# Kernel tuning notes

Measured on AMD Instinct MI355X. Metric: run time of the kernel, lower is better.

Reference implementation:

```python
import jax, jax.numpy as jnp
import numpy as np

B, T, F, H = 32, 1024, 128, 256
NUM_LAYERS = 3  # 2 return_sequences LSTMs + final LSTM


def setup_inputs() -> dict:
    key = jax.random.key(0)
    ks = jax.random.split(key, 2 + 3 * NUM_LAYERS + 2)
    x = jax.random.normal(ks[0], (B, 2, T, F), jnp.float32)
    # ragged lengths: pad tail with zeros (Masking(mask_value=0) semantics)
    lengths = jax.random.randint(ks[1], (B, 2), T // 4, T + 1)
    tmask = (jnp.arange(T)[None, None, :] < lengths[:, :, None]).astype(jnp.float32)
    x = x * tmask[..., None]
    inp = {"inputs": x}
    in_dims = [F] + [H] * (NUM_LAYERS - 1)
    for i, d in enumerate(in_dims):
        k = 2 + 3 * i
        inp[f"W{i}"] = jax.random.normal(ks[k], (d, 4 * H), jnp.float32) * (1.0 / np.sqrt(d))
        inp[f"U{i}"] = jax.random.normal(ks[k + 1], (H, 4 * H), jnp.float32) * (1.0 / np.sqrt(H))
        b = jnp.zeros((4 * H,), jnp.float32)
        inp[f"b{i}"] = b.at[H:2 * H].set(1.0)  # keras unit_forget_bias
    inp["dense_w"] = jax.random.normal(ks[-2], (1, 1), jnp.float32)
    inp["dense_b"] = jnp.zeros((1,), jnp.float32)
    return inp


def lstm_layer(x, mask, W, U, b):
    """Keras-style masked LSTM. x: [B,T,D], mask: [B,T] bool.
    Masked steps carry previous h/c and previous output (keras K.rnn masking).
    Gate order i,f,g,o; sigmoid recurrent activation, tanh activation."""
    xT = jnp.swapaxes(x, 0, 1)                  # [T,B,D]
    mT = jnp.swapaxes(mask, 0, 1)[..., None]    # [T,B,1]
    bsz, hd = x.shape[0], U.shape[0]
    h0 = jnp.zeros((bsz, hd), x.dtype)

    def step(carry, inp):
        h, c = carry
        x_t, m = inp
        z = x_t @ W + h @ U + b                 # [B,4H]
        i, f, g, o = jnp.split(z, 4, axis=-1)
        c_new = jax.nn.sigmoid(f) * c + jax.nn.sigmoid(i) * jnp.tanh(g)
        h_new = jax.nn.sigmoid(o) * jnp.tanh(c_new)
        h = jnp.where(m, h_new, h)
        c = jnp.where(m, c_new, c)
        return (h, c), h

    (h_final, _), ys = jax.lax.scan(step, (h0, h0), (xT, mT))
    return jnp.swapaxes(ys, 0, 1), h_final


def encode(x, Ws, Us, bs):
    mask = jnp.any(x != 0, axis=-1)             # Masking(mask_value=0)
    for W, U, b in zip(Ws[:-1], Us[:-1], bs[:-1]):
        x, _ = lstm_layer(x, mask, W, U, b)     # dropout is identity at inference
    _, h = lstm_layer(x, mask, Ws[-1], Us[-1], bs[-1])
    return h


def reference(inputs, W0, U0, b0, W1, U1, b1, W2, U2, b2, dense_w, dense_b):
    Ws, Us, bs = [W0, W1, W2], [U0, U1, U2], [b0, b1, b2]
    h1 = encode(inputs[:, 0], Ws, Us, bs)
    h2 = encode(inputs[:, 1], Ws, Us, bs)
    dist = jnp.linalg.norm(h1 - h2, axis=1, keepdims=True)   # [B,1]
    dist = jnp.clip(dist, 1e-7, 1e7)
    return jax.nn.sigmoid(dist @ dense_w + dense_b)          # [B,1]
```

## Files before the change

### kernel.cpp

```cpp
#include <hip/hip_runtime.h>


typedef __attribute__((ext_vector_type(8))) short bf16x8;
typedef __attribute__((ext_vector_type(4))) float f32x4;
typedef __attribute__((ext_vector_type(4))) unsigned int u32x4;
typedef unsigned long long ull;

__device__ __forceinline__ unsigned short f2bf(float f){
    unsigned u = __float_as_uint(f);
    u += 0x7FFFu + ((u >> 16) & 1u);
    return (unsigned short)(u >> 16);
}
__device__ __forceinline__ float fsig(float x){
    return __builtin_amdgcn_rcpf(1.0f + __expf(-x));
}
__device__ __forceinline__ float ftanh(float x){
    float e = __expf(-2.0f * fabsf(x));
    return copysignf((1.0f - e) * __builtin_amdgcn_rcpf(1.0f + e), x);
}
__device__ __forceinline__ ull ald(const ull* p){
    return __hip_atomic_load(p, __ATOMIC_RELAXED, __HIP_MEMORY_SCOPE_AGENT);
}
__device__ __forceinline__ void ast(unsigned int* p, unsigned int v){
    __hip_atomic_store(p, v, __ATOMIC_RELAXED, __HIP_MEMORY_SCOPE_AGENT);
}
__device__ __forceinline__ void st_pair(ull* p, ull v){
    asm volatile("global_store_dwordx2 %0, %1, off sc1" :: "v"((ull)p), "v"(v) : "memory");
}
__device__ __forceinline__ void st_plain(ull* p, ull v){
    asm volatile("global_store_dwordx2 %0, %1, off" :: "v"((ull)p), "v"(v) : "memory");
}
__device__ __forceinline__ int min16(const ull* p){
    int m = 0x7FFFFFFF;
    #pragma unroll
    for (int i = 0; i < 8; ++i){
        ull v = ald(p + i);
        m = min(m, min((int)(unsigned)v, (int)(v >> 32)));
    }
    return m;
}

#define POLL4_SC1(P, Q0,Q1,Q2,Q3)                                        \
  asm volatile("global_load_dwordx4 %0, %4, off sc1\n\t"                 \
               "global_load_dwordx4 %1, %4, off offset:1024 sc1\n\t"     \
               "global_load_dwordx4 %2, %4, off offset:2048 sc1\n\t"     \
               "global_load_dwordx4 %3, %4, off offset:3072 sc1"         \
               : "=&v"(Q0),"=&v"(Q1),"=&v"(Q2),"=&v"(Q3)                 \
               : "v"(P) : "memory")
#define POLL4_SC0(P, Q0,Q1,Q2,Q3)                                        \
  asm volatile("global_load_dwordx4 %0, %4, off sc0\n\t"                 \
               "global_load_dwordx4 %1, %4, off offset:1024 sc0\n\t"     \
               "global_load_dwordx4 %2, %4, off offset:2048 sc0\n\t"     \
               "global_load_dwordx4 %3, %4, off offset:3072 sc0"         \
               : "=&v"(Q0),"=&v"(Q1),"=&v"(Q2),"=&v"(Q3)                 \
               : "v"(P) : "memory")
#define PLAIN4(P, O0,O1,O2,O3)                                           \
  asm volatile("global_load_dwordx4 %0, %4, off\n\t"                     \
               "global_load_dwordx4 %1, %4, off offset:1024\n\t"         \
               "global_load_dwordx4 %2, %4, off offset:2048\n\t"         \
               "global_load_dwordx4 %3, %4, off offset:3072"             \
               : "=&v"(O0),"=&v"(O1),"=&v"(O2),"=&v"(O3)                 \
               : "v"(P) : "memory")

__device__ __forceinline__ ull pk(u32x4 q){
    return (((ull)(unsigned)q.z) << 32) | (unsigned)q.x;
}

template<bool FAST>
__device__ __forceinline__ void poll_tile(const char* tile, unsigned tg, int half,
                                          unsigned int* buf, int lane){
    const ull b0 = (ull)(tile + lane * 16 + half * 8192);
    u32x4 q0,q1,q2,q3,q4,q5,q6,q7;
    int spins = 0;
    for (;;){
        if (FAST){
            POLL4_SC0(b0,        q0, q1, q2, q3);
            POLL4_SC0(b0 + 4096, q4, q5, q6, q7);
        } else {
            POLL4_SC1(b0,        q0, q1, q2, q3);
            POLL4_SC1(b0 + 4096, q4, q5, q6, q7);
        }
        asm volatile("s_waitcnt vmcnt(0)" ::: "memory");
        __builtin_amdgcn_sched_barrier(0);
        bool ok = (q0.y==tg)&(q0.w==tg)&(q1.y==tg)&(q1.w==tg)
                & (q2.y==tg)&(q2.w==tg)&(q3.y==tg)&(q3.w==tg)
                & (q4.y==tg)&(q4.w==tg)&(q5.y==tg)&(q5.w==tg)
                & (q6.y==tg)&(q6.w==tg)&(q7.y==tg)&(q7.w==tg);
        if (__all(ok)) break;
        if (((++spins) & 15) == 0) __builtin_amdgcn_s_sleep(1);
    }
    ull* d = (ull*)buf + (half * 16 + (lane >> 5)) * 36 + (lane & 31);
    d[0]       = pk(q0); d[72]      = pk(q1); d[2 * 72]  = pk(q2); d[3 * 72] = pk(q3);
    d[4 * 72]  = pk(q4); d[5 * 72]  = pk(q5); d[6 * 72]  = pk(q6); d[7 * 72] = pk(q7);
}

__device__ __forceinline__ bf16x8 ldfrag(const unsigned int* buf, int r, int l15){
    return *(const bf16x8*)(buf + r * 72 + l15 * 4);
}

__device__ __forceinline__ bool probe_quad(ull* pb, ull nonce, int n){
    st_plain(pb + n, nonce);
    for (int it = 0; it < 400; ++it){
        ull a0, a1, a2, a3;
        asm volatile("global_load_dwordx2 %0, %4, off sc0\n\t"
                     "global_load_dwordx2 %1, %4, off offset:8 sc0\n\t"
                     "global_load_dwordx2 %2, %4, off offset:16 sc0\n\t"
                     "global_load_dwordx2 %3, %4, off offset:24 sc0\n\t"
                     "s_waitcnt vmcnt(0)"
                     : "=&v"(a0),"=&v"(a1),"=&v"(a2),"=&v"(a3)
                     : "v"((ull)pb) : "memory");
        if (a0 == nonce && a1 == nonce && a2 == nonce && a3 == nonce) return true;
        __builtin_amdgcn_s_sleep(2);
    }
    return false;
}
__device__ __forceinline__ bool consensus(ull* vd, ull nonce, int n, bool seen){
    st_pair(vd + n, (nonce << 1) | (seen ? 1ull : 0ull));
    for (;;){
        ull a0, a1, a2, a3;
        asm volatile("global_load_dwordx2 %0, %4, off sc1\n\t"
                     "global_load_dwordx2 %1, %4, off offset:8 sc1\n\t"
                     "global_load_dwordx2 %2, %4, off offset:16 sc1\n\t"
                     "global_load_dwordx2 %3, %4, off offset:24 sc1\n\t"
                     "s_waitcnt vmcnt(0)"
                     : "=&v"(a0),"=&v"(a1),"=&v"(a2),"=&v"(a3)
                     : "v"((ull)vd) : "memory");
        if ((a0 >> 1) == nonce && (a1 >> 1) == nonce &&
            (a2 >> 1) == nonce && (a3 >> 1) == nonce)
            return (a0 & a1 & a2 & a3 & 1ull) != 0;
        __builtin_amdgcn_s_sleep(1);
    }
}

__global__ void prep_kernel(const float* __restrict__ x, unsigned int* __restrict__ xb,
                            unsigned int* __restrict__ mb, unsigned* __restrict__ epoch){
    const int s = blockIdx.x, c = blockIdx.y, l = threadIdx.x;
    if (s == 0 && c == 0 && l == 0) atomicAdd(epoch, 1u);
    const int g = s >> 4, sg = s & 15;
    const int woff = ((l >> 4) * 4 + ((l >> 2) & 3)) * 64 + sg * 4 + (l & 3);
    const float* xs = x + ((size_t)s * 1024 + (size_t)c * 64) * 128;
    unsigned int w0 = 0, w1 = 0;
    for (int tt = 0; tt < 64; ++tt){
        const float2 v = *(const float2*)(xs + (size_t)tt * 128 + 2 * l);
        bool nz = (v.x != 0.0f) || (v.y != 0.0f);
        unsigned long long b = __ballot(nz);
        if (b){ if (tt < 32) w0 |= 1u << tt; else w1 |= 1u << (tt - 32); }
        unsigned int p = (unsigned)f2bf(v.x) | ((unsigned)f2bf(v.y) << 16);
        xb[((size_t)(c * 64 + tt) * 4 + g) * 1024 + woff] = p;
    }
    if (l == 0){ mb[s * 32 + c * 2] = w0; mb[s * 32 + c * 2 + 1] = w1; }
}

template<int LAYER>
__device__ __forceinline__ void scan_layer(
    int g, int n,
    const unsigned int* __restrict__ xb0,
    const ull* xin,
    ull* sring,
    ull* xout,
    const float* __restrict__ W, const float* __restrict__ U, const float* __restrict__ Bv,
    const unsigned int* __restrict__ mb,
    float* __restrict__ hfinal,
    int* prog, ull* probe, ull* verd, unsigned ep)
{
    constexpr int DK = (LAYER == 0) ? 4 : 8;
    constexpr int KT = DK + 8;
    const int lg = LAYER * 4 + g;
    const int tid  = threadIdx.x;
    const int w    = tid >> 6;
    const int lane = tid & 63;
    const int l15  = lane & 15, lk = lane >> 4;
    const int up   = lane & 7,  s2 = lane >> 3;

    __shared__ unsigned int hbuf[2][32 * 72];
    __shared__ unsigned int xbuf[2][32 * 72];
    __shared__ float zw[4][16][68];
    __shared__ unsigned int mbL[16][32];
    __shared__ int sgl, sFast;
    if (tid == 0) sgl = 0;
    for (int i = tid; i < 512; i += 256)
        mbL[i >> 5][i & 31] = mb[(g * 16 + (i >> 5)) * 32 + (i & 31)];
    __syncthreads();
    if (tid < 16){
        int last = 0;
        #pragma unroll
        for (int q = 0; q < 32; ++q){
            unsigned v = mbL[tid][q];
            if (v) last = q * 32 + (32 - __clz(v));
        }
        atomicMax(&sgl, last);
    }

    float bfr[4]; int gcol[4];
    #pragma unroll
    for (int nt = 0; nt < 4; ++nt){
        int lc = w * 64 + nt * 16 + l15;
        gcol[nt] = (lc & 3) * 256 + n * 64 + (lc >> 2);
        bfr[nt] = Bv[gcol[nt]];
    }
    bf16x8 Bf[KT][4];
    #pragma unroll
    for (int kt = 0; kt < KT; ++kt){
        const float* src = (kt < DK) ? (W + (size_t)(kt * 32 + lk * 8) * 1024)
                                     : (U + (size_t)((kt - DK) * 32 + lk * 8) * 1024);
        #pragma unroll
        for (int nt = 0; nt < 4; ++nt){
            bf16x8 v;
            #pragma unroll
            for (int j = 0; j < 8; ++j) v[j] = (short)f2bf(src[(size_t)j * 1024 + gcol[nt]]);
            Bf[kt][nt] = v;
        }
    }
    if (tid == 0){
        ull nonce = (((ull)ep) << 8) | 0xA5u;
        bool seen = probe_quad(probe + (size_t)lg * 8, nonce, n);
        sFast = consensus(verd + (size_t)lg * 8, nonce, n, seen) ? 1 : 0;
    }
    __syncthreads();
    const int gl = sgl;
    const bool fast = (sFast != 0);

    const int hhalf = (w == 0) ? 0 : (w == 2) ? 1 : -1;
    const int xhalf = (w == 1) ? 0 : (w == 3) ? 1 : -1;

    float c00 = 0, c01 = 0, c10 = 0, c11 = 0;
    float h00 = 0, h01 = 0, h10 = 0, h11 = 0;
    const int hcol = n * 32 + w * 8 + up;
    const int woff0 = ((hcol >> 4) * 4 + ((hcol >> 2) & 3)) * 64 + s2 * 4 + (hcol & 3);
    ull xv0p = 0, xv1p = 0; int tprev = -1;

    for (int t = 0; t < gl; ++t){
        if (LAYER > 0 && (t & 31) == 0 && lane == 0)
            ast((unsigned*)(prog + (LAYER - 1) * 64 + g * 16 + n * 4 + w), (unsigned)t);
        if (LAYER < 2 && (t & 31) == 0){
            const ull* pp = (const ull*)(prog + LAYER * 64 + g * 16);
            int spins = 0;
            while (min16(pp) < t - 96)
                if (((++spins) & 15) == 0) __builtin_amdgcn_s_sleep(1);
        }

        unsigned int* hbL = &hbuf[t & 1][0];
        unsigned int* xbL = &xbuf[t & 1][0];
        if (t > 0 && hhalf >= 0){
            const char* tile = (const char*)sring + (((size_t)((t - 1) & 7) * 4 + g) * 16384);
            if (fast) poll_tile<true >(tile, (unsigned)t, hhalf, hbL, lane);
            else      poll_tile<false>(tile, (unsigned)t, hhalf, hbL, lane);
        }
        if (LAYER > 0 && xhalf >= 0)
            poll_tile<false>((const char*)xin + (((size_t)(t & 127) * 4 + g) * 16384),
                             (unsigned)(t + 1), xhalf, xbL, lane);
        __syncthreads();

        f32x4 acc[4];
        #pragma unroll
        for (int nt = 0; nt < 4; ++nt) acc[nt] = (f32x4){bfr[nt], bfr[nt], bfr[nt], bfr[nt]};
        if (LAYER == 0){
            u32x4 xq0, xq1, xq2, xq3;
            ull xaddr = (ull)((const char*)(xb0 + ((size_t)t * 4 + g) * 1024) + lane * 16);
            PLAIN4(xaddr, xq0, xq1, xq2, xq3);
            asm volatile("s_waitcnt vmcnt(0)" ::: "memory");
            __builtin_amdgcn_sched_barrier(0);
            if (tprev >= 0){
                ull* xd = xout + ((size_t)(tprev & 127) * 4 + g) * 2048 + woff0;
                st_pair(xd, xv0p); st_pair(xd + 32, xv1p);
            }
            bf16x8 a0 = __builtin_bit_cast(bf16x8, xq0);
            bf16x8 a1 = __builtin_bit_cast(bf16x8, xq1);
            bf16x8 a2 = __builtin_bit_cast(bf16x8, xq2);
            bf16x8 a3 = __builtin_bit_cast(bf16x8, xq3);
            #pragma unroll
            for (int nt = 0; nt < 4; ++nt){
                acc[nt] = __builtin_amdgcn_mfma_f32_16x16x32_bf16(a0, Bf[0][nt], acc[nt], 0, 0, 0);
                acc[nt] = __builtin_amdgcn_mfma_f32_16x16x32_bf16(a1, Bf[1][nt], acc[nt], 0, 0, 0);
                acc[nt] = __builtin_amdgcn_mfma_f32_16x16x32_bf16(a2, Bf[2][nt], acc[nt], 0, 0, 0);
                acc[nt] = __builtin_amdgcn_mfma_f32_16x16x32_bf16(a3, Bf[3][nt], acc[nt], 0, 0, 0);
            }
        } else {
            if (LAYER == 1 && tprev >= 0){
                ull* xd = xout + ((size_t)(tprev & 127) * 4 + g) * 2048 + woff0;
                st_pair(xd, xv0p); st_pair(xd + 32, xv1p);
            }
            #pragma unroll
            for (int kt = 0; kt < 8; ++kt){
                bf16x8 a = ldfrag(xbL, kt * 4 + lk, l15);
                #pragma unroll
                for (int nt = 0; nt < 4; ++nt)
                    acc[nt] = __builtin_amdgcn_mfma_f32_16x16x32_bf16(a, Bf[kt][nt], acc[nt], 0, 0, 0);
            }
        }
        if (t > 0){
            #pragma unroll
            for (int kh = 0; kh < 8; ++kh){
                bf16x8 a = ldfrag(hbL, kh * 4 + lk, l15);
                #pragma unroll
                for (int nt = 0; nt < 4; ++nt)
                    acc[nt] = __builtin_amdgcn_mfma_f32_16x16x32_bf16(a, Bf[DK + kh][nt], acc[nt], 0, 0, 0);
            }
        }
        #pragma unroll
        for (int nt = 0; nt < 4; ++nt)
            #pragma unroll
            for (int r = 0; r < 4; ++r)
                zw[w][lk * 4 + r][nt * 16 + l15] = acc[nt][r];
        asm volatile("s_waitcnt lgkmcnt(0)" ::: "memory");
        __builtin_amdgcn_sched_barrier(0);

        bool m0 = (mbL[s2][t >> 5]     >> (t & 31)) & 1;
        bool m1 = (mbL[s2 + 8][t >> 5] >> (t & 31)) & 1;
        const float* z0 = &zw[w][s2][up * 8];
        const float* z1 = &zw[w][s2 + 8][up * 8];
        float cn, hn;
        cn = fsig(z0[1]) * c00 + fsig(z0[0]) * ftanh(z0[2]); hn = fsig(z0[3]) * ftanh(cn);
        if (m0){ c00 = cn; h00 = hn; }
        cn = fsig(z0[5]) * c01 + fsig(z0[4]) * ftanh(z0[6]); hn = fsig(z0[7]) * ftanh(cn);
        if (m0){ c01 = cn; h01 = hn; }
        cn = fsig(z1[1]) * c10 + fsig(z1[0]) * ftanh(z1[2]); hn = fsig(z1[3]) * ftanh(cn);
        if (m1){ c10 = cn; h10 = hn; }
        cn = fsig(z1[5]) * c11 + fsig(z1[4]) * ftanh(z1[6]); hn = fsig(z1[7]) * ftanh(cn);
        if (m1){ c11 = cn; h11 = hn; }

        unsigned p0 = (unsigned)f2bf(h00) | ((unsigned)f2bf(h01) << 16);
        unsigned p1 = (unsigned)f2bf(h10) | ((unsigned)f2bf(h11) << 16);
        ull tg = ((ull)(unsigned)(t + 1)) << 32;
        ull v0 = (ull)p0 | tg, v1 = (ull)p1 | tg;
        ull* sdst = sring + ((size_t)(t & 7) * 4 + g) * 2048 + woff0;
        if (fast){ st_plain(sdst, v0); st_plain(sdst + 32, v1); }
        else     { st_pair (sdst, v0); st_pair (sdst + 32, v1); }
        if (LAYER < 2){ xv0p = v0; xv1p = v1; tprev = t; }
    }

    if (LAYER < 2 && tprev >= 0){
        ull* xd = xout + ((size_t)(tprev & 127) * 4 + g) * 2048 + woff0;
        st_pair(xd, xv0p); st_pair(xd + 32, xv1p);
    }
    if (LAYER > 0 && lane == 0)
        ast((unsigned*)(prog + (LAYER - 1) * 64 + g * 16 + n * 4 + w), 0x40000000u);

    if (LAYER == 2){
        const int colb = n * 64 + w * 16 + up * 2;
        const int myseq0 = g * 16 + s2, myseq1 = g * 16 + s2 + 8;
        hfinal[(size_t)myseq0 * 256 + colb]     = h00;
        hfinal[(size_t)myseq0 * 256 + colb + 1] = h01;
        hfinal[(size_t)myseq1 * 256 + colb]     = h10;
        hfinal[(size_t)myseq1 * 256 + colb + 1] = h11;
    }
}

__global__ __launch_bounds__(256, 1) void scan3_kernel(
    const unsigned int* xb, ull* x01, ull* x12, ull* s0, ull* s1, ull* s2,
    const float* W0, const float* U0, const float* b0,
    const float* W1, const float* U1, const float* b1,
    const float* W2, const float* U2, const float* b2,
    const unsigned int* mb, int* prog, unsigned* epoch,
    ull* probe, ull* verd, float* hfinal)
{
    const int xcd = blockIdx.x & 7, slot = blockIdx.x >> 3;
    const int q = xcd + 8 * (slot >> 2);
    if (q >= 12) return;
    const int n = slot & 3;
    const int layer = q >> 2, g = q & 3;
    const unsigned ep = *epoch;
    if (layer == 0)
        scan_layer<0>(g, n, xb, nullptr, s0, x01, W0, U0, b0, mb, nullptr, prog, probe, verd, ep);
    else if (layer == 1)
        scan_layer<1>(g, n, nullptr, x01, s1, x12, W1, U1, b1, mb, nullptr, prog, probe, verd, ep);
    else
        scan_layer<2>(g, n, nullptr, x12, s2, nullptr, W2, U2, b2, mb, hfinal, prog, probe, verd, ep);
}

__global__ void final_kernel(const float* __restrict__ hfinal, const float* __restrict__ dw,
                             const float* __restrict__ db, float* __restrict__ out){
    const int b = threadIdx.x >> 3, j = threadIdx.x & 7;
    const float* ha = hfinal + (size_t)(2 * b) * 256;
    const float* hb = ha + 256;
    float s = 0.0f;
    for (int d = j; d < 256; d += 8){ float df = ha[d] - hb[d]; s += df * df; }
    #pragma unroll
    for (int off = 4; off; off >>= 1) s += __shfl_xor(s, off, 8);
    if (j == 0){
        float dist = sqrtf(s);
        dist = fminf(fmaxf(dist, 1e-7f), 1e7f);
        out[b] = fsig(dist * dw[0] + db[0]);
    }
}

extern "C" void kernel_launch(void* const* d_in, const int* in_sizes, int n_in,
                              void* d_out, int out_size, void* d_ws, size_t ws_size,
                              hipStream_t stream){
    const float* x  = (const float*)d_in[0];
    const float* W0 = (const float*)d_in[1];
    const float* U0 = (const float*)d_in[2];
    const float* b0 = (const float*)d_in[3];
    const float* W1 = (const float*)d_in[4];
    const float* U1 = (const float*)d_in[5];
    const float* b1 = (const float*)d_in[6];
    const float* W2 = (const float*)d_in[7];
    const float* U2 = (const float*)d_in[8];
    const float* b2 = (const float*)d_in[9];
    const float* dw = (const float*)d_in[10];
    const float* db = (const float*)d_in[11];

    char* ws = (char*)d_ws;
    unsigned int* xb     = (unsigned int*)(ws);
    ull*          x01    = (ull*)(ws + 16777216ull);
    ull*          x12    = (ull*)(ws + 25165824ull);
    ull*          s0     = (ull*)(ws + 33554432ull);
    ull*          s1     = (ull*)(ws + 34078720ull);
    ull*          s2     = (ull*)(ws + 34603008ull);
    int*          prog   = (int*)(ws + 35127296ull);
    unsigned*     epoch  = (unsigned*)(ws + 35127808ull);
    ull*          probe  = (ull*)(ws + 35128320ull);
    ull*          verd   = (ull*)(ws + 35129088ull);
    unsigned int* mb     = (unsigned int*)(ws + 35131392ull);
    float*        hfinal = (float*)(ws + 35139584ull);
    float*        out    = (float*)d_out;

    (void)hipMemsetAsync(ws + 35127296ull, 0, 512, stream);

    prep_kernel<<<dim3(64, 16), 64, 0, stream>>>(x, xb, mb, epoch);
    scan3_kernel<<<64, 256, 0, stream>>>(xb, x01, x12, s0, s1, s2,
                                         W0, U0, b0, W1, U1, b1, W2, U2, b2,
                                         mb, prog, epoch, probe, verd, hfinal);
    final_kernel<<<1, 256, 0, stream>>>(hfinal, dw, db, out);
}
```

Baseline: 2.720 ms.

## Swap MFMA operands so gate math stays in registers and tag each bf16 word

The MFMA operands are swapped so each lane's accumulator holds the i,f,g,o gates for one hidden unit. The LSTM cell update now runs straight from registers, which drops the zw shared-memory round trip and its lgkm wait. Hidden-state publication changes from 64-bit pairs tagged with a 32-bit step to 32-bit words that each carry one bf16 value and a 16-bit step tag. Pollers now detag into a transposed shared layout [16][264], and the layer-0 x prefetch is issued before polling. In exchange, the published data carries more tag overhead, there are more scattered 2-byte LDS writes, and the 16-bit tag could wrap on longer sequences.

```diff
diff --git a/kernel.cpp b/kernel.cpp
--- a/kernel.cpp
+++ b/kernel.cpp
@@ -27,8 +27,14 @@
 __device__ __forceinline__ void st_pair(ull* p, ull v){
     asm volatile("global_store_dwordx2 %0, %1, off sc1" :: "v"((ull)p), "v"(v) : "memory");
 }
-__device__ __forceinline__ void st_plain(ull* p, ull v){
+__device__ __forceinline__ void st_plain8(ull* p, ull v){
     asm volatile("global_store_dwordx2 %0, %1, off" :: "v"((ull)p), "v"(v) : "memory");
+}
+__device__ __forceinline__ void stw_sc1(unsigned* p, unsigned v){
+    asm volatile("global_store_dword %0, %1, off sc1" :: "v"((ull)p), "v"(v) : "memory");
+}
+__device__ __forceinline__ void stw_plain(unsigned* p, unsigned v){
+    asm volatile("global_store_dword %0, %1, off" :: "v"((ull)p), "v"(v) : "memory");
 }
 __device__ __forceinline__ int min16(const ull* p){
     int m = 0x7FFFFFFF;
@@ -62,14 +68,15 @@
                : "=&v"(O0),"=&v"(O1),"=&v"(O2),"=&v"(O3)                 \
                : "v"(P) : "memory")
 
-__device__ __forceinline__ ull pk(u32x4 q){
-    return (((ull)(unsigned)q.z) << 32) | (unsigned)q.x;
+__device__ __forceinline__ bool tagsok(u32x4 q, unsigned tg){
+    return ((q.x >> 16) == tg) && ((q.y >> 16) == tg) &&
+           ((q.z >> 16) == tg) && ((q.w >> 16) == tg);
 }
 
 template<bool FAST>
 __device__ __forceinline__ void poll_tile(const char* tile, unsigned tg, int half,
-                                          unsigned int* buf, int lane){
-    const ull b0 = (ull)(tile + lane * 16 + half * 8192);
+                                          unsigned short (*buf)[264], int lane){
+    const ull b0 = (ull)(tile + half * 8192 + lane * 16);
     u32x4 q0,q1,q2,q3,q4,q5,q6,q7;
     int spins = 0;
     for (;;){
@@ -82,24 +89,25 @@
         }
         asm volatile("s_waitcnt vmcnt(0)" ::: "memory");
         __builtin_amdgcn_sched_barrier(0);
-        bool ok = (q0.y==tg)&(q0.w==tg)&(q1.y==tg)&(q1.w==tg)
-                & (q2.y==tg)&(q2.w==tg)&(q3.y==tg)&(q3.w==tg)
-                & (q4.y==tg)&(q4.w==tg)&(q5.y==tg)&(q5.w==tg)
-                & (q6.y==tg)&(q6.w==tg)&(q7.y==tg)&(q7.w==tg);
+        bool ok = tagsok(q0, tg) & tagsok(q1, tg) & tagsok(q2, tg) & tagsok(q3, tg)
+                & tagsok(q4, tg) & tagsok(q5, tg) & tagsok(q6, tg) & tagsok(q7, tg);
         if (__all(ok)) break;
         if (((++spins) & 15) == 0) __builtin_amdgcn_s_sleep(1);
     }
-    ull* d = (ull*)buf + (half * 16 + (lane >> 5)) * 36 + (lane & 31);
-    d[0]       = pk(q0); d[72]      = pk(q1); d[2 * 72]  = pk(q2); d[3 * 72] = pk(q3);
-    d[4 * 72]  = pk(q4); d[5 * 72]  = pk(q5); d[6 * 72]  = pk(q6); d[7 * 72] = pk(q7);
-}
-
-__device__ __forceinline__ bf16x8 ldfrag(const unsigned int* buf, int r, int l15){
-    return *(const bf16x8*)(buf + r * 72 + l15 * 4);
+    const int hb = half * 128 + (lane >> 2);
+    const int sb = (lane & 3) * 4;
+#define DETAG(Q, IT) { int hh = hb + (IT)*16;                     \
+    buf[sb+0][hh] = (unsigned short)(Q).x;                        \
+    buf[sb+1][hh] = (unsigned short)(Q).y;                        \
+    buf[sb+2][hh] = (unsigned short)(Q).z;                        \
+    buf[sb+3][hh] = (unsigned short)(Q).w; }
+    DETAG(q0,0) DETAG(q1,1) DETAG(q2,2) DETAG(q3,3)
+    DETAG(q4,4) DETAG(q5,5) DETAG(q6,6) DETAG(q7,7)
+#undef DETAG
 }
 
 __device__ __forceinline__ bool probe_quad(ull* pb, ull nonce, int n){
-    st_plain(pb + n, nonce);
+    st_plain8(pb + n, nonce);
     for (int it = 0; it < 400; ++it){
         ull a0, a1, a2, a3;
         asm volatile("global_load_dwordx2 %0, %4, off sc0\n\t"
@@ -155,9 +163,9 @@
 __device__ __forceinline__ void scan_layer(
     int g, int n,
     const unsigned int* __restrict__ xb0,
-    const ull* xin,
-    ull* sring,
-    ull* xout,
+    const unsigned int* xin,
+    unsigned int* sring,
+    unsigned int* xout,
     const float* __restrict__ W, const float* __restrict__ U, const float* __restrict__ Bv,
     const unsigned int* __restrict__ mb,
     float* __restrict__ hfinal,
@@ -170,11 +178,9 @@
     const int w    = tid >> 6;
     const int lane = tid & 63;
     const int l15  = lane & 15, lk = lane >> 4;
-    const int up   = lane & 7,  s2 = lane >> 3;
-
-    __shared__ unsigned int hbuf[2][32 * 72];
-    __shared__ unsigned int xbuf[2][32 * 72];
-    __shared__ float zw[4][16][68];
+
+    __shared__ unsigned short hT[2][16][264];
+    __shared__ unsigned short xT[2][16][264];
     __shared__ unsigned int mbL[16][32];
     __shared__ int sgl, sFast;
     if (tid == 0) sgl = 0;
@@ -191,13 +197,18 @@
         atomicMax(&sgl, last);
     }
 
-    float bfr[4]; int gcol[4];
+    int gcol[4];
     #pragma unroll
     for (int nt = 0; nt < 4; ++nt){
         int lc = w * 64 + nt * 16 + l15;
         gcol[nt] = (lc & 3) * 256 + n * 64 + (lc >> 2);
-        bfr[nt] = Bv[gcol[nt]];
-    }
+    }
+    float bfr2[4][4];
+    #pragma unroll
+    for (int nt = 0; nt < 4; ++nt)
+        #pragma unroll
+        for (int r = 0; r < 4; ++r)
+            bfr2[nt][r] = Bv[r * 256 + n * 64 + w * 16 + nt * 4 + lk];
     bf16x8 Bf[KT][4];
     #pragma unroll
     for (int kt = 0; kt < KT; ++kt){
@@ -223,11 +234,9 @@
     const int hhalf = (w == 0) ? 0 : (w == 2) ? 1 : -1;
     const int xhalf = (w == 1) ? 0 : (w == 3) ? 1 : -1;
 
-    float c00 = 0, c01 = 0, c10 = 0, c11 = 0;
-    float h00 = 0, h01 = 0, h10 = 0, h11 = 0;
-    const int hcol = n * 32 + w * 8 + up;
-    const int woff0 = ((hcol >> 4) * 4 + ((hcol >> 2) & 3)) * 64 + s2 * 4 + (hcol & 3);
-    ull xv0p = 0, xv1p = 0; int tprev = -1;
+    float cs[4] = {0, 0, 0, 0}, hs[4] = {0, 0, 0, 0};
+    const int pubbase = (n * 64 + w * 16) * 16 + lane;
+    unsigned xv[4]; int tprev = -1;
 
     for (int t = 0; t < gl; ++t){
         if (LAYER > 0 && (t & 31) == 0 && lane == 0)
@@ -239,115 +248,111 @@
                 if (((++spins) & 15) == 0) __builtin_amdgcn_s_sleep(1);
         }
 
-        unsigned int* hbL = &hbuf[t & 1][0];
-        unsigned int* xbL = &xbuf[t & 1][0];
+        u32x4 xq0, xq1, xq2, xq3;
+        if (LAYER == 0){
+            ull xaddr = (ull)((const char*)(xb0 + ((size_t)t * 4 + g) * 1024) + lane * 16);
+            PLAIN4(xaddr, xq0, xq1, xq2, xq3);
+        }
+        const int p = t & 1;
         if (t > 0 && hhalf >= 0){
             const char* tile = (const char*)sring + (((size_t)((t - 1) & 7) * 4 + g) * 16384);
-            if (fast) poll_tile<true >(tile, (unsigned)t, hhalf, hbL, lane);
-            else      poll_tile<false>(tile, (unsigned)t, hhalf, hbL, lane);
+            if (fast) poll_tile<true >(tile, (unsigned)t, hhalf, hT[p], lane);
+            else      poll_tile<false>(tile, (unsigned)t, hhalf, hT[p], lane);
         }
         if (LAYER > 0 && xhalf >= 0)
             poll_tile<false>((const char*)xin + (((size_t)(t & 127) * 4 + g) * 16384),
-                             (unsigned)(t + 1), xhalf, xbL, lane);
+                             (unsigned)(t + 1), xhalf, xT[p], lane);
         __syncthreads();
-
-        f32x4 acc[4];
-        #pragma unroll
-        for (int nt = 0; nt < 4; ++nt) acc[nt] = (f32x4){bfr[nt], bfr[nt], bfr[nt], bfr[nt]};
         if (LAYER == 0){
-            u32x4 xq0, xq1, xq2, xq3;
-            ull xaddr = (ull)((const char*)(xb0 + ((size_t)t * 4 + g) * 1024) + lane * 16);
-            PLAIN4(xaddr, xq0, xq1, xq2, xq3);
             asm volatile("s_waitcnt vmcnt(0)" ::: "memory");
             __builtin_amdgcn_sched_barrier(0);
-            if (tprev >= 0){
-                ull* xd = xout + ((size_t)(tprev & 127) * 4 + g) * 2048 + woff0;
-                st_pair(xd, xv0p); st_pair(xd + 32, xv1p);
-            }
-            bf16x8 a0 = __builtin_bit_cast(bf16x8, xq0);
-            bf16x8 a1 = __builtin_bit_cast(bf16x8, xq1);
-            bf16x8 a2 = __builtin_bit_cast(bf16x8, xq2);
-            bf16x8 a3 = __builtin_bit_cast(bf16x8, xq3);
+        }
+
+        if (LAYER < 2 && tprev >= 0){
+            unsigned* xd = xout + ((size_t)(tprev & 127) * 4 + g) * 4096 + pubbase;
+            #pragma unroll
+            for (int nt = 0; nt < 4; ++nt) stw_sc1(xd + nt * 64, xv[nt]);
+            __builtin_amdgcn_sched_barrier(0);
+        }
+
+        f32x4 acc[4];
+        #pragma unroll
+        for (int nt = 0; nt < 4; ++nt)
+            acc[nt] = (f32x4){bfr2[nt][0], bfr2[nt][1], bfr2[nt][2], bfr2[nt][3]};
+        if (LAYER == 0){
+            bf16x8 b0 = __builtin_bit_cast(bf16x8, xq0);
+            bf16x8 b1 = __builtin_bit_cast(bf16x8, xq1);
+            bf16x8 b2 = __builtin_bit_cast(bf16x8, xq2);
+            bf16x8 b3 = __builtin_bit_cast(bf16x8, xq3);
             #pragma unroll
             for (int nt = 0; nt < 4; ++nt){
-                acc[nt] = __builtin_amdgcn_mfma_f32_16x16x32_bf16(a0, Bf[0][nt], acc[nt], 0, 0, 0);
-                acc[nt] = __builtin_amdgcn_mfma_f32_16x16x32_bf16(a1, Bf[1][nt], acc[nt], 0, 0, 0);
-                acc[nt] = __builtin_amdgcn_mfma_f32_16x16x32_bf16(a2, Bf[2][nt], acc[nt], 0, 0, 0);
-                acc[nt] = __builtin_amdgcn_mfma_f32_16x16x32_bf16(a3, Bf[3][nt], acc[nt], 0, 0, 0);
+                acc[nt] = __builtin_amdgcn_mfma_f32_16x16x32_bf16(Bf[0][nt], b0, acc[nt], 0, 0, 0);
+                acc[nt] = __builtin_amdgcn_mfma_f32_16x16x32_bf16(Bf[1][nt], b1, acc[nt], 0, 0, 0);
+                acc[nt] = __builtin_amdgcn_mfma_f32_16x16x32_bf16(Bf[2][nt], b2, acc[nt], 0, 0, 0);
+                acc[nt] = __builtin_amdgcn_mfma_f32_16x16x32_bf16(Bf[3][nt], b3, acc[nt], 0, 0, 0);
             }
         } else {
-            if (LAYER == 1 && tprev >= 0){
-                ull* xd = xout + ((size_t)(tprev & 127) * 4 + g) * 2048 + woff0;
-                st_pair(xd, xv0p); st_pair(xd + 32, xv1p);
-            }
             #pragma unroll
             for (int kt = 0; kt < 8; ++kt){
-                bf16x8 a = ldfrag(xbL, kt * 4 + lk, l15);
+                bf16x8 b = *(const bf16x8*)(&xT[p][l15][kt * 32 + lk * 8]);
                 #pragma unroll
                 for (int nt = 0; nt < 4; ++nt)
-                    acc[nt] = __builtin_amdgcn_mfma_f32_16x16x32_bf16(a, Bf[kt][nt], acc[nt], 0, 0, 0);
+                    acc[nt] = __builtin_amdgcn_mfma_f32_16x16x32_bf16(Bf[kt][nt], b, acc[nt], 0, 0, 0);
             }
         }
         if (t > 0){
             #pragma unroll
-            for (int kh = 0; kh < 8; ++kh){
-                bf16x8 a = ldfrag(hbL, kh * 4 + lk, l15);
+            for (int kk = 0; kk < 8; ++kk){
+                bf16x8 b = *(const bf16x8*)(&hT[p][l15][kk * 32 + lk * 8]);
                 #pragma unroll
                 for (int nt = 0; nt < 4; ++nt)
-                    acc[nt] = __builtin_amdgcn_mfma_f32_16x16x32_bf16(a, Bf[DK + kh][nt], acc[nt], 0, 0, 0);
+                    acc[nt] = __builtin_amdgcn_mfma_f32_16x16x32_bf16(Bf[DK + kk][nt], b, acc[nt], 0, 0, 0);
             }
         }
-        #pragma unroll
-        for (int nt = 0; nt < 4; ++nt)
-            #pragma unroll
-            for (int r = 0; r < 4; ++r)
-                zw[w][lk * 4 + r][nt * 16 + l15] = acc[nt][r];
-        asm volatile("s_waitcnt lgkmcnt(0)" ::: "memory");
-        __builtin_amdgcn_sched_barrier(0);
-
-        bool m0 = (mbL[s2][t >> 5]     >> (t & 31)) & 1;
-        bool m1 = (mbL[s2 + 8][t >> 5] >> (t & 31)) & 1;
-        const float* z0 = &zw[w][s2][up * 8];
-        const float* z1 = &zw[w][s2 + 8][up * 8];
-        float cn, hn;
-        cn = fsig(z0[1]) * c00 + fsig(z0[0]) * ftanh(z0[2]); hn = fsig(z0[3]) * ftanh(cn);
-        if (m0){ c00 = cn; h00 = hn; }
-        cn = fsig(z0[5]) * c01 + fsig(z0[4]) * ftanh(z0[6]); hn = fsig(z0[7]) * ftanh(cn);
-        if (m0){ c01 = cn; h01 = hn; }
-        cn = fsig(z1[1]) * c10 + fsig(z1[0]) * ftanh(z1[2]); hn = fsig(z1[3]) * ftanh(cn);
-        if (m1){ c10 = cn; h10 = hn; }
-        cn = fsig(z1[5]) * c11 + fsig(z1[4]) * ftanh(z1[6]); hn = fsig(z1[7]) * ftanh(cn);
-        if (m1){ c11 = cn; h11 = hn; }
-
-        unsigned p0 = (unsigned)f2bf(h00) | ((unsigned)f2bf(h01) << 16);
-        unsigned p1 = (unsigned)f2bf(h10) | ((unsigned)f2bf(h11) << 16);
-        ull tg = ((ull)(unsigned)(t + 1)) << 32;
-        ull v0 = (ull)p0 | tg, v1 = (ull)p1 | tg;
-        ull* sdst = sring + ((size_t)(t & 7) * 4 + g) * 2048 + woff0;
-        if (fast){ st_plain(sdst, v0); st_plain(sdst + 32, v1); }
-        else     { st_pair (sdst, v0); st_pair (sdst + 32, v1); }
-        if (LAYER < 2){ xv0p = v0; xv1p = v1; tprev = t; }
+        asm volatile("s_waitcnt vmcnt(0)" ::: "memory");
+
+        bool m = (mbL[l15][t >> 5] >> (t & 31)) & 1;
+        #pragma unroll
+        for (int nt = 0; nt < 4; ++nt){
+            float i_ = acc[nt][0], f_ = acc[nt][1], g_ = acc[nt][2], o_ = acc[nt][3];
+            float cn = fsig(f_) * cs[nt] + fsig(i_) * ftanh(g_);
+            float hn = fsig(o_) * ftanh(cn);
+            if (m){ cs[nt] = cn; hs[nt] = hn; }
+        }
+
+        unsigned tg = ((unsigned)(t + 1)) << 16;
+        unsigned v0 = (unsigned)f2bf(hs[0]) | tg, v1 = (unsigned)f2bf(hs[1]) | tg;
+        unsigned v2 = (unsigned)f2bf(hs[2]) | tg, v3 = (unsigned)f2bf(hs[3]) | tg;
+        unsigned* sd = sring + ((size_t)(t & 7) * 4 + g) * 4096 + pubbase;
+        if (fast){
+            stw_plain(sd, v0); stw_plain(sd + 64, v1);
+            stw_plain(sd + 128, v2); stw_plain(sd + 192, v3);
+        } else {
+            stw_sc1(sd, v0); stw_sc1(sd + 64, v1);
+            stw_sc1(sd + 128, v2); stw_sc1(sd + 192, v3);
+        }
+        if (LAYER < 2){ xv[0] = v0; xv[1] = v1; xv[2] = v2; xv[3] = v3; tprev = t; }
     }
 
     if (LAYER < 2 && tprev >= 0){
-        ull* xd = xout + ((size_t)(tprev & 127) * 4 + g) * 2048 + woff0;
-        st_pair(xd, xv0p); st_pair(xd + 32, xv1p);
+        unsigned* xd = xout + ((size_t)(tprev & 127) * 4 + g) * 4096 + pubbase;
+        #pragma unroll
+        for (int nt = 0; nt < 4; ++nt) stw_sc1(xd + nt * 64, xv[nt]);
     }
     if (LAYER > 0 && lane == 0)
         ast((unsigned*)(prog + (LAYER - 1) * 64 + g * 16 + n * 4 + w), 0x40000000u);
 
     if (LAYER == 2){
-        const int colb = n * 64 + w * 16 + up * 2;
-        const int myseq0 = g * 16 + s2, myseq1 = g * 16 + s2 + 8;
-        hfinal[(size_t)myseq0 * 256 + colb]     = h00;
-        hfinal[(size_t)myseq0 * 256 + colb + 1] = h01;
-        hfinal[(size_t)myseq1 * 256 + colb]     = h10;
-        hfinal[(size_t)myseq1 * 256 + colb + 1] = h11;
+        const int seqg = g * 16 + l15;
+        #pragma unroll
+        for (int nt = 0; nt < 4; ++nt)
+            hfinal[(size_t)seqg * 256 + n * 64 + w * 16 + nt * 4 + lk] = hs[nt];
     }
 }
 
 __global__ __launch_bounds__(256, 1) void scan3_kernel(
-    const unsigned int* xb, ull* x01, ull* x12, ull* s0, ull* s1, ull* s2,
+    const unsigned int* xb, unsigned int* x01, unsigned int* x12,
+    unsigned int* s0, unsigned int* s1, unsigned int* s2,
     const float* W0, const float* U0, const float* b0,
     const float* W1, const float* U1, const float* b1,
     const float* W2, const float* U2, const float* b2,
@@ -380,7 +385,7 @@
     if (j == 0){
         float dist = sqrtf(s);
         dist = fminf(fmaxf(dist, 1e-7f), 1e7f);
-        out[b] = fsig(dist * dw[0] + db[0]);
+        out[b] = 1.0f / (1.0f + __expf(-(dist * dw[0] + db[0])));
     }
 }
 
@@ -402,11 +407,11 @@
 
     char* ws = (char*)d_ws;
     unsigned int* xb     = (unsigned int*)(ws);
-    ull*          x01    = (ull*)(ws + 16777216ull);
-    ull*          x12    = (ull*)(ws + 25165824ull);
-    ull*          s0     = (ull*)(ws + 33554432ull);
-    ull*          s1     = (ull*)(ws + 34078720ull);
-    ull*          s2     = (ull*)(ws + 34603008ull);
+    unsigned int* x01    = (unsigned int*)(ws + 16777216ull);
+    unsigned int* x12    = (unsigned int*)(ws + 25165824ull);
+    unsigned int* s0     = (unsigned int*)(ws + 33554432ull);
+    unsigned int* s1     = (unsigned int*)(ws + 34078720ull);
+    unsigned int* s2     = (unsigned int*)(ws + 34603008ull);
     int*          prog   = (int*)(ws + 35127296ull);
     unsigned*     epoch  = (unsigned*)(ws + 35127808ull);
     ull*          probe  = (ull*)(ws + 35128320ull);
```

Result: slower. 3.283 ms (+20.7%).
